# Performance work log

Hardware: AMD Instinct MI355X
Metric: run time of the kernel (lower is better)

Reference implementation:

```python
import jax, jax.numpy as jnp
import numpy as np

D = 1024  # d_model

def setup_inputs() -> dict:
    key = jax.random.key(0)
    ks = jax.random.split(key, 12)
    s = 1.0 / np.sqrt(D)  # torch Linear default init scale
    inp = {
        "q": jax.random.normal(ks[0], (4, 4096, D), dtype=jnp.float32),
        "k": jax.random.normal(ks[1], (4, 4096, D), dtype=jnp.float32),
        "v": jax.random.normal(ks[2], (4, 4096, D), dtype=jnp.float32),
        "Wq": jax.random.uniform(ks[3], (D, D), jnp.float32, -s, s),
        "bq": jax.random.uniform(ks[4], (D,), jnp.float32, -s, s),
        "Wk": jax.random.uniform(ks[5], (D, D), jnp.float32, -s, s),
        "bk": jax.random.uniform(ks[6], (D,), jnp.float32, -s, s),
        "Wv": jax.random.uniform(ks[7], (D, D), jnp.float32, -s, s),
        "bv": jax.random.uniform(ks[8], (D,), jnp.float32, -s, s),
        "Wo": jax.random.uniform(ks[9], (D, D), jnp.float32, -s, s),
        "bo": jax.random.uniform(ks[10], (D,), jnp.float32, -s, s),
    }
    return inp

def reference(q, k, v, Wq, bq, Wk, bk, Wv, bv, Wo, bo):
    # phi feature map: exp(-x^2 / 2)
    phi = lambda x: jnp.exp(-0.5 * x * x)
    Q = phi(q @ Wq.T + bq)            # [B, N, D]
    K = phi(k @ Wk.T + bk)            # [B, N, D]
    V = v @ Wv.T + bv                 # [B, N, D]
    # linear attention: aggregate K^T V once, then contract with Q
    KV = jnp.einsum('bnd,bnl->bdl', K, V)                 # [B, D, D]
    Z = 1.0 / (jnp.einsum('bnd,bd->bn', Q, K.sum(axis=1)) + 1e-6)  # [B, N]
    out = jnp.einsum('bnd,bdl->bnl', Q, KV) * Z[..., None]         # [B, N, D]
    return out @ Wo.T + bo
```

## Files before the change

kernel.cpp:

```cpp
#include <hip/hip_runtime.h>

typedef unsigned short u16;
typedef unsigned int u32;
typedef unsigned long long u64;

typedef __attribute__((ext_vector_type(8))) short short8;
typedef __attribute__((ext_vector_type(4))) float floatx4;

__device__ __forceinline__ float b2f(u16 h) {
  u32 u = ((u32)h) << 16;
  return __builtin_bit_cast(float, u);
}
__device__ __forceinline__ u16 f2b(float f) {
  u32 u = __builtin_bit_cast(u32, f);
  u32 r = 0x7FFFu + ((u >> 16) & 1u);
  return (u16)((u + r) >> 16);
}

__device__ __forceinline__ void gl_lds16(const void* g, void* l) {
  __builtin_amdgcn_global_load_lds(
      (__attribute__((address_space(1))) void*)(u64)g,
      (__attribute__((address_space(3))) void*)(u32)(u64)l, 16, 0, 0);
}

enum { EPI_PHI_BIAS = 0, EPI_BIAS = 1, EPI_NONE = 2,
       EPI_ZBIAS_F32 = 3 };

template<int EPI, bool TRANS_OUT, bool A_F32>
__global__ __launch_bounds__(512, 2)
void gemm_bt256(const void* __restrict__ Ap, const u16* __restrict__ Bp0,
                const float* __restrict__ bias, const float* __restrict__ Zall,
                void* __restrict__ Cp,
                int M, int N, int K, int ldA, int ldB, int ldC,
                long sAb, long sBb, long sCb, long sZb, int abmask, int kshift)
{
  constexpr int TSTRIDE = 65536;
  constexpr int BOFF    = 32768;
  __shared__ char smem[2 * TSTRIDE];

  const int tid  = threadIdx.x;
  const int lane = tid & 63;
  const int wave = tid >> 6;
  const int wm = wave >> 2, wn = wave & 3;
  const int fl = lane & 15;
  const int q  = lane >> 4;
  const int r4 = q * 4;
  const int bm0 = blockIdx.x * 256, bn0 = blockIdx.y * 256;
  const int bz = blockIdx.z;
  const int abz = bz & abmask;
  const int kbase = (bz >> kshift) * K;

  const u16*   Ah = (const u16*)Ap   + (size_t)abz * sAb + kbase;
  const float* Af = (const float*)Ap + (size_t)abz * sAb + kbase;
  const u16*   Bh = Bp0 + (size_t)abz * sBb + kbase;

  const u16* gA[4]; const float* gAf[4]; const u16* gB[4]; int sL[4], dL[4];
  #pragma unroll
  for (int n = 0; n < 4; ++n) {
    int j = n * 512 + tid;
    int R = j >> 3, c = (j & 7) ^ (R & 7);
    if constexpr (A_F32) gAf[n] = Af + (size_t)(bm0 + R) * ldA + c * 8;
    else                 gA[n]  = Ah + (size_t)(bm0 + R) * ldA + c * 8;
    gB[n] = Bh + (size_t)(bn0 + R) * ldB + c * 8;
    sL[n] = (n * 512 + wave * 64) * 16;
    dL[n] = j * 16;
  }

  int aoff[8], boff[4];
  #pragma unroll
  for (int i = 0; i < 8; ++i) {
    int ra = wm * 128 + i * 16 + fl;
    aoff[i] = ra * 128 + ((q ^ (ra & 7)) * 16);
  }
  #pragma unroll
  for (int i = 0; i < 4; ++i) {
    int rb = wn * 64 + i * 16 + fl;
    boff[i] = rb * 128 + ((q ^ (rb & 7)) * 16);
  }

  floatx4 zero = {0.f, 0.f, 0.f, 0.f};
  floatx4 acc[8][4];
  #pragma unroll
  for (int i = 0; i < 8; ++i)
    #pragma unroll
    for (int j = 0; j < 4; ++j) acc[i][j] = zero;

  auto stageB = [&](int t, char* base) {
    #pragma unroll
    for (int n = 0; n < 4; ++n) gl_lds16(gB[n] + t * 64, base + BOFF + sL[n]);
  };
  auto stageA_dma = [&](int t, char* base) {
    #pragma unroll
    for (int n = 0; n < 4; ++n) gl_lds16(gA[n] + t * 64, base + sL[n]);
  };

  float4 rA[8];
  auto loadA = [&](int t) {
    #pragma unroll
    for (int n = 0; n < 4; ++n) {
      rA[2 * n]     = *(const float4*)(gAf[n] + t * 64);
      rA[2 * n + 1] = *(const float4*)(gAf[n] + t * 64 + 4);
    }
  };
  auto packA = [&](char* base) {
    #pragma unroll
    for (int n = 0; n < 4; ++n) {
      const u32* xb = (const u32*)&rA[2 * n];
      const u32* yb = (const u32*)&rA[2 * n + 1];
      union { u32 w[4]; short8 s; } cv;
      cv.w[0] = __builtin_amdgcn_perm(xb[1], xb[0], 0x07060302u);
      cv.w[1] = __builtin_amdgcn_perm(xb[3], xb[2], 0x07060302u);
      cv.w[2] = __builtin_amdgcn_perm(yb[1], yb[0], 0x07060302u);
      cv.w[3] = __builtin_amdgcn_perm(yb[3], yb[2], 0x07060302u);
      *(short8*)(base + dL[n]) = cv.s;
    }
  };

  auto kstep = [&](const char* bufc, int xo) {
    short8 bF[4], aF[8];
    #pragma unroll
    for (int i = 0; i < 4; ++i) bF[i] = *(const short8*)(bufc + BOFF + (boff[i] ^ xo));
    #pragma unroll
    for (int i = 0; i < 8; ++i) aF[i] = *(const short8*)(bufc + (aoff[i] ^ xo));
    __builtin_amdgcn_s_setprio(1);
    #pragma unroll
    for (int mi = 0; mi < 8; ++mi)
      #pragma unroll
      for (int ni = 0; ni < 4; ++ni)
        acc[mi][ni] = __builtin_amdgcn_mfma_f32_16x16x32_bf16(
            aF[mi], bF[ni], acc[mi][ni], 0, 0, 0);
    __builtin_amdgcn_s_setprio(0);
  };

  const int NT = K >> 6;
  if constexpr (A_F32) {
    loadA(0); stageB(0, smem);
    asm volatile("s_waitcnt vmcnt(4)" ::: "memory");
    packA(smem);
    asm volatile("s_waitcnt vmcnt(0) lgkmcnt(0)\ns_barrier" ::: "memory");
    int cur = 0;
    for (int t = 0; t < NT; ++t) {
      const bool pf = t + 1 < NT;
      const char* bufc = smem + cur;
      char* bufn = smem + (cur ^ TSTRIDE);
      if (pf) { loadA(t + 1); stageB(t + 1, bufn); }
      kstep(bufc, 0);
      if (pf) packA(bufn);
      kstep(bufc, 64);
      if (pf)
        asm volatile("s_waitcnt vmcnt(0) lgkmcnt(0)\ns_barrier" ::: "memory");
      cur ^= TSTRIDE;
    }
  } else {
    stageA_dma(0, smem); stageB(0, smem);
    asm volatile("s_waitcnt vmcnt(0)\ns_barrier" ::: "memory");
    int cur = 0;
    for (int t = 0; t < NT; ++t) {
      if (t + 1 < NT) {
        stageA_dma(t + 1, smem + (cur ^ TSTRIDE));
        stageB(t + 1, smem + (cur ^ TSTRIDE));
      }
      const char* bufc = smem + cur;
      kstep(bufc, 0);
      kstep(bufc, 64);
      if (t + 1 < NT)
        asm volatile("s_waitcnt vmcnt(0) lgkmcnt(0)\ns_barrier" ::: "memory");
      cur ^= TSTRIDE;
    }
  }

  if constexpr (!TRANS_OUT) {
    #pragma unroll
    for (int mi = 0; mi < 8; ++mi) {
      #pragma unroll
      for (int ni = 0; ni < 4; ++ni) {
        int col = bn0 + wn * 64 + ni * 16 + fl;
        #pragma unroll
        for (int r = 0; r < 4; ++r) {
          int row = bm0 + wm * 128 + mi * 16 + r4 + r;
          float vv = acc[mi][ni][r];
          if constexpr (EPI == EPI_PHI_BIAS) {
            vv += bias[col];
            vv = __expf(-0.5f * vv * vv);
          }
          if constexpr (EPI == EPI_ZBIAS_F32)
            vv = vv * Zall[(size_t)abz * sZb + row] + bias[col];
          if constexpr (EPI == EPI_ZBIAS_F32)
            ((float*)Cp)[(size_t)bz * sCb + (size_t)row * ldC + col] = vv;
          else
            ((u16*)Cp)[(size_t)bz * sCb + (size_t)row * ldC + col] = f2b(vv);
        }
      }
    }
  } else {
    u16* sT = (u16*)smem;
    #pragma unroll
    for (int p = 0; p < 2; ++p) {
      __syncthreads();
      if ((wn >> 1) == p) {
        #pragma unroll
        for (int mi = 0; mi < 8; ++mi) {
          #pragma unroll
          for (int ni = 0; ni < 4; ++ni) {
            int colL = wn * 64 + ni * 16 + fl;
            int row0 = wm * 128 + mi * 16 + r4;
            float bcol = bias[bn0 + colL];
            ushort4 h;
            #pragma unroll
            for (int r = 0; r < 4; ++r) {
              float vv = acc[mi][ni][r] + bcol;
              if constexpr (EPI == EPI_PHI_BIAS) vv = __expf(-0.5f * vv * vv);
              ((u16*)&h)[r] = f2b(vv);
            }
            *(ushort4*)(sT + (colL - p * 128) * 264 + row0) = h;
          }
        }
      }
      __syncthreads();
      #pragma unroll
      for (int i = 0; i < 8; ++i) {
        int c = tid + i * 512;
        int dloc = c >> 5, t8 = (c & 31) * 8;
        int4 vv = *(const int4*)(sT + dloc * 264 + t8);
        int gd = bn0 + p * 128 + dloc;
        int gt = bm0 + t8;
        int batch = gt >> 12, tt = gt & 4095;
        *(int4*)((u16*)Cp + ((size_t)batch * N + gd) * 4096 + tt) = vv;
      }
    }
  }
}

__global__ __launch_bounds__(256)
void wconv(const float* __restrict__ w0, const float* __restrict__ w1,
           const float* __restrict__ w2, const float* __restrict__ w3,
           u16* __restrict__ dst) {
  unsigned e = blockIdx.x * 256 + threadIdx.x;
  int mat = e >> 18;
  size_t off = (size_t)(e & 262143) * 4;
  const float* src = mat == 0 ? w0 : mat == 1 ? w1 : mat == 2 ? w2 : w3;
  float4 v = *(const float4*)(src + off);
  ushort4 h;
  h.x = f2b(v.x); h.y = f2b(v.y); h.z = f2b(v.z); h.w = f2b(v.w);
  *(ushort4*)(dst + (size_t)mat * 1048576 + off) = h;
}

__global__ __launch_bounds__(256)
void reduce4(const u16* __restrict__ P, u16* __restrict__ out) {
  size_t i = ((size_t)blockIdx.x * 256 + threadIdx.x) * 8;
  int4 a = *(const int4*)(P + i);
  int4 b = *(const int4*)(P + i + 4194304);
  int4 c = *(const int4*)(P + i + 8388608);
  int4 d = *(const int4*)(P + i + 12582912);
  const u16* ha = (const u16*)&a; const u16* hb = (const u16*)&b;
  const u16* hc = (const u16*)&c; const u16* hd = (const u16*)&d;
  ushort4 o0, o1;
  #pragma unroll
  for (int j = 0; j < 8; ++j) {
    float s = b2f(ha[j]) + b2f(hb[j]) + b2f(hc[j]) + b2f(hd[j]);
    ((u16*)(j < 4 ? &o0 : &o1))[j & 3] = f2b(s);
  }
  *(ushort4*)(out + i) = o0;
  *(ushort4*)(out + i + 4) = o1;
}

__global__ __launch_bounds__(256)
void ksum_rows(const u16* __restrict__ KT, float* __restrict__ Ksum) {
  int lane = threadIdx.x & 63;
  int row = blockIdx.x * 4 + (threadIdx.x >> 6);
  const u16* p = KT + (size_t)row * 4096;
  float s = 0.f;
  #pragma unroll
  for (int i = 0; i < 8; ++i) {
    int4 d = *(const int4*)(p + i * 512 + lane * 8);
    const u16* h = (const u16*)&d;
    #pragma unroll
    for (int j = 0; j < 8; ++j) s += b2f(h[j]);
  }
  #pragma unroll
  for (int off = 32; off; off >>= 1) s += __shfl_xor(s, off, 64);
  if (lane == 0) Ksum[row] = s;
}

__global__ __launch_bounds__(256)
void zden(const u16* __restrict__ Qb, const float* __restrict__ Ksum,
          float* __restrict__ Z) {
  int lane = threadIdx.x & 63;
  int t = blockIdx.x * 4 + (threadIdx.x >> 6);
  const u16* qp = Qb + (size_t)t * 1024;
  const float* ks = Ksum + (size_t)(t >> 12) * 1024;
  float s = 0.f;
  #pragma unroll
  for (int i = 0; i < 2; ++i) {
    int idx = i * 512 + lane * 8;
    int4 d = *(const int4*)(qp + idx);
    const u16* h = (const u16*)&d;
    float4 k0 = *(const float4*)(ks + idx);
    float4 k1 = *(const float4*)(ks + idx + 4);
    s += b2f(h[0]) * k0.x + b2f(h[1]) * k0.y + b2f(h[2]) * k0.z + b2f(h[3]) * k0.w
       + b2f(h[4]) * k1.x + b2f(h[5]) * k1.y + b2f(h[6]) * k1.z + b2f(h[7]) * k1.w;
  }
  #pragma unroll
  for (int off = 32; off; off >>= 1) s += __shfl_xor(s, off, 64);
  if (lane == 0) Z[t] = 1.0f / (s + 1e-6f);
}

extern "C" void kernel_launch(void* const* d_in, const int* in_sizes, int n_in,
                              void* d_out, int out_size, void* d_ws, size_t ws_size,
                              hipStream_t stream) {
  const float* q  = (const float*)d_in[0];
  const float* k  = (const float*)d_in[1];
  const float* v  = (const float*)d_in[2];
  const float* Wq = (const float*)d_in[3];
  const float* bq = (const float*)d_in[4];
  const float* Wk = (const float*)d_in[5];
  const float* bk = (const float*)d_in[6];
  const float* Wv = (const float*)d_in[7];
  const float* bv = (const float*)d_in[8];
  const float* Wo = (const float*)d_in[9];
  const float* bo = (const float*)d_in[10];
  float* out = (float*)d_out;

  u16* Wqb = (u16*)d_ws;
  u16* Wkb = Wqb + 1048576;
  u16* Wvb = Wkb + 1048576;
  u16* Wob = Wvb + 1048576;
  u16* Qb  = Wob + 1048576;
  u16* KT  = Qb  + 16777216;
  u16* VT  = KT  + 16777216;
  u16* KVr = VT  + 16777216;
  float* Ksum = (float*)(KVr + 4194304);
  float* Z    = Ksum + 4096;
  u16* Pkv = Qb;
  u16* Pg  = VT;
  u16* Gp  = KT;

  wconv<<<4096, 256, 0, stream>>>(Wq, Wk, Wv, Wo, Wqb);

  dim3 gp(64, 4, 1);
  gemm_bt256<EPI_PHI_BIAS, true, true><<<gp, 512, 0, stream>>>(
      k, Wkb, bk, nullptr, KT, 16384, 1024, 1024, 1024, 1024, 0,
      0, 0, 0, 0, 0, 2);
  ksum_rows<<<1024, 256, 0, stream>>>(KT, Ksum);

  gemm_bt256<EPI_BIAS, true, true><<<gp, 512, 0, stream>>>(
      v, Wvb, bv, nullptr, VT, 16384, 1024, 1024, 1024, 1024, 0,
      0, 0, 0, 0, 0, 2);

  dim3 g2(4, 4, 16);
  gemm_bt256<EPI_NONE, false, false><<<g2, 512, 0, stream>>>(
      KT, VT, nullptr, nullptr, Pkv, 1024, 1024, 1024, 4096, 4096, 1024,
      4194304L, 4194304L, 1048576L, 0, 3, 2);
  reduce4<<<2048, 256, 0, stream>>>(Pkv, KVr);

  dim3 gg(4, 4, 16);
  gemm_bt256<EPI_NONE, false, false><<<gg, 512, 0, stream>>>(
      Wob, KVr, nullptr, nullptr, Pg, 1024, 1024, 256, 1024, 1024, 1024,
      0L, 1048576L, 1048576L, 0, 3, 2);
  reduce4<<<2048, 256, 0, stream>>>(Pg, Gp);

  gemm_bt256<EPI_PHI_BIAS, false, true><<<gp, 512, 0, stream>>>(
      q, Wqb, bq, nullptr, Qb, 16384, 1024, 1024, 1024, 1024, 1024,
      0, 0, 0, 0, 0, 2);
  zden<<<4096, 256, 0, stream>>>(Qb, Ksum, Z);

  dim3 gf(16, 4, 4);
  gemm_bt256<EPI_ZBIAS_F32, false, false><<<gf, 512, 0, stream>>>(
      Qb, Gp, bo, Z, out, 4096, 1024, 1024, 1024, 1024, 1024,
      4194304L, 1048576L, 4194304L, 4096L, 3, 2);
}
```

Baseline: 289.2 us.

## Prefetch fp32 A tiles two steps ahead with double-buffered registers

The fp32 A operand is now loaded into one of two register buffers two k-steps ahead. The pack into LDS happens after both MFMA half-steps, and the wait drops to vmcnt(8) so the newest A loads can stay in flight across the barrier. This aims to hide global load latency for the fp32 A path behind more compute. The cost is 32 more VGPRs for the second buffer, which could reduce occupancy or cause spills, and the vmcnt accounting depends on load ordering.

```diff
diff --git a/kernel.cpp b/kernel.cpp
--- a/kernel.cpp
+++ b/kernel.cpp
@@ -94,28 +94,6 @@
     for (int n = 0; n < 4; ++n) gl_lds16(gA[n] + t * 64, base + sL[n]);
   };
 
-  float4 rA[8];
-  auto loadA = [&](int t) {
-    #pragma unroll
-    for (int n = 0; n < 4; ++n) {
-      rA[2 * n]     = *(const float4*)(gAf[n] + t * 64);
-      rA[2 * n + 1] = *(const float4*)(gAf[n] + t * 64 + 4);
-    }
-  };
-  auto packA = [&](char* base) {
-    #pragma unroll
-    for (int n = 0; n < 4; ++n) {
-      const u32* xb = (const u32*)&rA[2 * n];
-      const u32* yb = (const u32*)&rA[2 * n + 1];
-      union { u32 w[4]; short8 s; } cv;
-      cv.w[0] = __builtin_amdgcn_perm(xb[1], xb[0], 0x07060302u);
-      cv.w[1] = __builtin_amdgcn_perm(xb[3], xb[2], 0x07060302u);
-      cv.w[2] = __builtin_amdgcn_perm(yb[1], yb[0], 0x07060302u);
-      cv.w[3] = __builtin_amdgcn_perm(yb[3], yb[2], 0x07060302u);
-      *(short8*)(base + dL[n]) = cv.s;
-    }
-  };
-
   auto kstep = [&](const char* bufc, int xo) {
     short8 bF[4], aF[8];
     #pragma unroll
@@ -134,21 +112,52 @@
 
   const int NT = K >> 6;
   if constexpr (A_F32) {
-    loadA(0); stageB(0, smem);
-    asm volatile("s_waitcnt vmcnt(4)" ::: "memory");
-    packA(smem);
-    asm volatile("s_waitcnt vmcnt(0) lgkmcnt(0)\ns_barrier" ::: "memory");
+    float4 rA0[8], rA1[8];
+    auto loadA = [&](int t, float4* r) {
+      #pragma unroll
+      for (int n = 0; n < 4; ++n) {
+        r[2 * n]     = *(const float4*)(gAf[n] + t * 64);
+        r[2 * n + 1] = *(const float4*)(gAf[n] + t * 64 + 4);
+      }
+    };
+    auto packA = [&](const float4* r, char* base) {
+      #pragma unroll
+      for (int n = 0; n < 4; ++n) {
+        const u32* xb = (const u32*)&r[2 * n];
+        const u32* yb = (const u32*)&r[2 * n + 1];
+        union { u32 w[4]; short8 s; } cv;
+        cv.w[0] = __builtin_amdgcn_perm(xb[1], xb[0], 0x07060302u);
+        cv.w[1] = __builtin_amdgcn_perm(xb[3], xb[2], 0x07060302u);
+        cv.w[2] = __builtin_amdgcn_perm(yb[1], yb[0], 0x07060302u);
+        cv.w[3] = __builtin_amdgcn_perm(yb[3], yb[2], 0x07060302u);
+        *(short8*)(base + dL[n]) = cv.s;
+      }
+    };
+    loadA(0, rA0);
+    stageB(0, smem);
+    if (NT > 1) loadA(1, rA1);
+    packA(rA0, smem);
+    asm volatile("s_waitcnt vmcnt(8) lgkmcnt(0)\ns_barrier" ::: "memory");
     int cur = 0;
     for (int t = 0; t < NT; ++t) {
-      const bool pf = t + 1 < NT;
+      const bool pf1 = t + 1 < NT;
+      const bool pf2 = t + 2 < NT;
       const char* bufc = smem + cur;
       char* bufn = smem + (cur ^ TSTRIDE);
-      if (pf) { loadA(t + 1); stageB(t + 1, bufn); }
+      if (pf1) stageB(t + 1, bufn);
       kstep(bufc, 0);
-      if (pf) packA(bufn);
       kstep(bufc, 64);
-      if (pf)
-        asm volatile("s_waitcnt vmcnt(0) lgkmcnt(0)\ns_barrier" ::: "memory");
+      if (pf1) {
+        if ((t & 1) == 0) {
+          packA(rA1, bufn);
+          if (pf2) loadA(t + 2, rA0);
+        } else {
+          packA(rA0, bufn);
+          if (pf2) loadA(t + 2, rA1);
+        }
+        if (pf2) asm volatile("s_waitcnt vmcnt(8) lgkmcnt(0)\ns_barrier" ::: "memory");
+        else     asm volatile("s_waitcnt vmcnt(0) lgkmcnt(0)\ns_barrier" ::: "memory");
+      }
       cur ^= TSTRIDE;
     }
   } else {
```

Result: slower. 349.1 us (+20.7%).
